# Kernel optimization log

Hardware: AMD Instinct MI355X
Metric: run time of the kernel (lower is better)

Reference implementation:

```python
import jax, jax.numpy as jnp
import numpy as np

N_HEADS = 16
EMBD = 1024
D_HEAD = EMBD // N_HEADS

def setup_inputs() -> dict:
    key = jax.random.key(0)
    ks = jax.random.split(key, 5)
    x = jax.random.normal(ks[0], (2, 2048, EMBD), dtype=jnp.float32)
    # Linear weights stored torch-style [out, in]; apply as x @ W.T + b
    W_in = jax.random.normal(ks[1], (3 * EMBD, EMBD), dtype=jnp.float32) * (EMBD ** -0.5)
    b_in = jax.random.normal(ks[2], (3 * EMBD,), dtype=jnp.float32) * 0.01
    W_out = jax.random.normal(ks[3], (EMBD, EMBD), dtype=jnp.float32) * (EMBD ** -0.5)
    b_out = jax.random.normal(ks[4], (EMBD,), dtype=jnp.float32) * 0.01
    return {"x": x, "W_in": W_in, "b_in": b_in, "W_out": W_out, "b_out": b_out}

def reference(x, W_in, b_in, W_out, b_out):
    B, S, D = x.shape
    qkv = x @ W_in.T + b_in                      # [B, S, 3D]
    q, k, v = jnp.split(qkv, 3, axis=-1)
    def heads(t):
        return t.reshape(B, S, N_HEADS, D_HEAD).transpose(0, 2, 1, 3)  # [B,H,S,d]
    q, k, v = heads(q), heads(k), heads(v)
    scale = 1.0 / jnp.sqrt(jnp.float32(D_HEAD))
    scores = jnp.einsum('bhqd,bhkd->bhqk', q, k) * scale
    weights = jax.nn.softmax(scores, axis=-1)
    out = jnp.einsum('bhqk,bhkd->bhqd', weights, v)  # [B,H,S,d]
    out = out.transpose(0, 2, 1, 3).reshape(B, S, D)
    return out @ W_out.T + b_out
```

## Files before the change

### kernel.cpp

```cpp
#include <hip/hip_runtime.h>
#include <cstdint>

#define EMBD 1024
#define NH 16
#define DH 64
#define BB 2
#define SS 2048
#define M_TOT (BB*SS)
#define N_QKV (3*EMBD)

typedef __bf16 bf16_t;
typedef bf16_t bf16x8 __attribute__((ext_vector_type(8)));
typedef float f32x4 __attribute__((ext_vector_type(4)));
typedef unsigned short u16;
typedef unsigned int u32;

static __device__ __forceinline__ u16 f2bf(float f) {
    union { float f; unsigned u; } c; c.f = f;
    unsigned u = c.u;
    unsigned r = (u + 0x7FFFu + ((u >> 16) & 1u)) >> 16;
    return (u16)r;
}

#define GLDS16(gp, lp) \
    __builtin_amdgcn_global_load_lds((const __attribute__((address_space(1))) void*)(gp), \
                                     (__attribute__((address_space(3))) void*)(lp), 16, 0, 0)

#define NX8 (M_TOT * EMBD / 8)
#define NWI8 (N_QKV * EMBD / 8)
#define NWO8 (EMBD * EMBD / 8)
__global__ void cast_all(const float* __restrict__ x, const float* __restrict__ wi,
                         const float* __restrict__ wo, u16* __restrict__ xb,
                         u16* __restrict__ wib, u16* __restrict__ wob) {
    int i = blockIdx.x * blockDim.x + threadIdx.x;
    const float* s; u16* d; int off;
    if (i < NX8)              { s = x;  d = xb;  off = i; }
    else if (i < NX8 + NWI8)  { s = wi; d = wib; off = i - NX8; }
    else                      { s = wo; d = wob; off = i - NX8 - NWI8; }
    const float4* s4 = (const float4*)s;
    float4 a = s4[2 * off];
    float4 b = s4[2 * off + 1];
    union { u16 u[8]; uint4 v; } r;
    r.u[0] = f2bf(a.x); r.u[1] = f2bf(a.y); r.u[2] = f2bf(a.z); r.u[3] = f2bf(a.w);
    r.u[4] = f2bf(b.x); r.u[5] = f2bf(b.y); r.u[6] = f2bf(b.z); r.u[7] = f2bf(b.w);
    ((uint4*)d)[off] = r.v;
}

#define QSCALE (0.125f * 1.4426950408889634f)
__global__ __launch_bounds__(256) void gemm_qkv(
    const u16* __restrict__ Xb,
    const u16* __restrict__ Wb,
    const float* __restrict__ b_in,
    u16* __restrict__ Q, u16* __restrict__ Kf, u16* __restrict__ Vpf)
{
    __shared__ u16 AB[3][8192];
    const int t = threadIdx.x;
    const int lane = t & 63;
    const int wave = t >> 6;
    const int wm = wave >> 1, wn = wave & 1;
    const int quad = lane >> 4, l16 = lane & 15;
    const int m0 = blockIdx.y * 128, n0 = blockIdx.x * 128;

    const int s0i = t, s1i = 256 + t;
    const u16* ga0 = Xb + (size_t)(m0 + (s0i >> 2)) * EMBD + (s0i & 3) * 8;
    const u16* ga1 = Xb + (size_t)(m0 + (s1i >> 2)) * EMBD + (s1i & 3) * 8;
    const u16* gb0 = Wb + (size_t)(n0 + (s0i >> 2)) * EMBD + (s0i & 3) * 8;
    const u16* gb1 = Wb + (size_t)(n0 + (s1i >> 2)) * EMBD + (s1i & 3) * 8;

    f32x4 acc[4][4] = {};

#pragma unroll
    for (int p = 0; p < 2; ++p) {
        u16* buf = &AB[p][0];
        GLDS16(ga0 + p * 32, buf + s0i * 8);
        GLDS16(ga1 + p * 32, buf + s1i * 8);
        GLDS16(gb0 + p * 32, buf + 4096 + s0i * 8);
        GLDS16(gb1 + p * 32, buf + 4096 + s1i * 8);
    }

    int bi = 0;
    int bw = 2;
    for (int it = 0; it < EMBD / 32; ++it) {
        asm volatile("s_waitcnt vmcnt(4)" ::: "memory");
        __syncthreads();
        {
            int k0 = (it + 2) * 32;
            u16* buf = &AB[bw][0];
            GLDS16(ga0 + k0, buf + s0i * 8);
            GLDS16(ga1 + k0, buf + s1i * 8);
            GLDS16(gb0 + k0, buf + 4096 + s0i * 8);
            GLDS16(gb1 + k0, buf + 4096 + s1i * 8);
        }
        const u16* As = &AB[bi][0];
        const u16* Bs = &AB[bi][4096];
        bf16x8 af[4], bfr[4];
#pragma unroll
        for (int im = 0; im < 4; ++im)
            af[im] = *(const bf16x8*)(As + (wm * 64 + im * 16 + l16) * 32 + quad * 8);
#pragma unroll
        for (int in = 0; in < 4; ++in)
            bfr[in] = *(const bf16x8*)(Bs + (wn * 64 + in * 16 + l16) * 32 + quad * 8);
#pragma unroll
        for (int im = 0; im < 4; ++im)
#pragma unroll
            for (int in = 0; in < 4; ++in)
                acc[im][in] = __builtin_amdgcn_mfma_f32_16x16x32_bf16(
                    af[im], bfr[in], acc[im][in], 0, 0, 0);
        bi = (bi == 2) ? 0 : bi + 1;
        bw = (bw == 2) ? 0 : bw + 1;
    }

#pragma unroll
    for (int im = 0; im < 4; ++im) {
        int rbase = m0 + wm * 64 + im * 16 + quad * 4;
        int b = rbase >> 11, ss = rbase & (SS - 1);
#pragma unroll
        for (int in = 0; in < 4; ++in) {
            int col = n0 + wn * 64 + in * 16 + l16;
            float bias = b_in[col];
            float v0 = acc[im][in][0] + bias;
            float v1 = acc[im][in][1] + bias;
            float v2 = acc[im][in][2] + bias;
            float v3 = acc[im][in][3] + bias;
            if (col < EMBD) {
                int h = col >> 6, d = col & 63;
                u16* qp = Q + (((size_t)(b * NH + h) * SS) + ss) * DH + d;
                qp[0]      = f2bf(v0 * QSCALE);
                qp[DH]     = f2bf(v1 * QSCALE);
                qp[2 * DH] = f2bf(v2 * QSCALE);
                qp[3 * DH] = f2bf(v3 * QSCALE);
            } else if (col < 2 * EMBD) {
                int c = col - EMBD; int h = c >> 6, d = c & 63;
                u16* kp = Kf + (size_t)(b * NH + h) * SS * DH
                          + (ss >> 4) * 1024 + (d >> 5) * 512
                          + (ss & 15) * 32 + ((d >> 3) & 3) * 8 + (d & 7);
                kp[0]  = f2bf(v0);
                kp[32] = f2bf(v1);
                kp[64] = f2bf(v2);
                kp[96] = f2bf(v3);
            } else {
                int c = col - 2 * EMBD; int h = c >> 6, d = c & 63;
                int p32 = ((ss >> 2) & 3) * 8 + ((ss >> 4) & 1) * 4;
                u32 lo = (u32)f2bf(v0) | ((u32)f2bf(v1) << 16);
                u32 hi = (u32)f2bf(v2) | ((u32)f2bf(v3) << 16);
                uint2 pk; pk.x = lo; pk.y = hi;
                *(uint2*)(Vpf + (size_t)(b * NH + h) * SS * DH
                          + (ss >> 5) * 2048 + (d >> 4) * 512 + (d & 15) * 32 + p32) = pk;
            }
        }
    }
}

#define OST 72
__global__ __launch_bounds__(256, 2) void attn(
    const u16* __restrict__ Q, const u16* __restrict__ Kf,
    const u16* __restrict__ Vpf, u16* __restrict__ AO)
{
    __shared__ u16 KV[2][16384];
    const int t = threadIdx.x;
    const int lane = t & 63, w = t >> 6;
    const int quad = lane >> 4, l16 = lane & 15;
    const int b0 = blockIdx.x;
    const int bh = (b0 & 7) * 4 + ((b0 >> 3) & 3);
    const int qt = b0 >> 5;
    const int q0 = qt * 128 + w * 32;

    const u16* Qh = Q + ((size_t)bh * SS + q0) * DH;
    const u16* Kh = Kf + (size_t)bh * SS * DH;
    const u16* Vh = Vpf + (size_t)bh * SS * DH;

    bf16x8 qb[2][2];
#pragma unroll
    for (int qi = 0; qi < 2; ++qi) {
        qb[qi][0] = *(const bf16x8*)(Qh + (qi * 16 + l16) * DH + quad * 8);
        qb[qi][1] = *(const bf16x8*)(Qh + (qi * 16 + l16) * DH + 32 + quad * 8);
    }

    f32x4 o[2][4] = {};
    float lsum[2] = {0.f, 0.f};

#pragma unroll
    for (int i = 0; i < 4; ++i) {
        GLDS16(Kh + i * 2048 + t * 8, &KV[0][0] + i * 2048 + t * 8);
        GLDS16(Vh + i * 2048 + t * 8, &KV[0][8192] + i * 2048 + t * 8);
    }

    for (int it = 0; it < SS / 128; ++it) {
        asm volatile("s_waitcnt vmcnt(0)" ::: "memory");
        __syncthreads();
        if (it + 1 < SS / 128) {
            const u16* kc = Kh + (it + 1) * 8192;
            const u16* vc = Vh + (it + 1) * 8192;
            u16* kb = &KV[(it + 1) & 1][0];
            u16* vb = &KV[(it + 1) & 1][8192];
#pragma unroll
            for (int i = 0; i < 4; ++i) {
                GLDS16(kc + i * 2048 + t * 8, kb + i * 2048 + t * 8);
                GLDS16(vc + i * 2048 + t * 8, vb + i * 2048 + t * 8);
            }
        }
        const u16* Kb = &KV[it & 1][0];
        const u16* Vb = &KV[it & 1][8192];
#pragma unroll
        for (int g = 0; g < 4; ++g) {
            bf16x8 ka00 = *(const bf16x8*)(Kb + (2 * g) * 1024 +       l16 * 32 + quad * 8);
            bf16x8 ka01 = *(const bf16x8*)(Kb + (2 * g) * 1024 + 512 + l16 * 32 + quad * 8);
            bf16x8 ka10 = *(const bf16x8*)(Kb + (2 * g + 1) * 1024 +       l16 * 32 + quad * 8);
            bf16x8 ka11 = *(const bf16x8*)(Kb + (2 * g + 1) * 1024 + 512 + l16 * 32 + quad * 8);
            bf16x8 va0 = *(const bf16x8*)(Vb + g * 2048 +        l16 * 32 + quad * 8);
            bf16x8 va1 = *(const bf16x8*)(Vb + g * 2048 + 512  + l16 * 32 + quad * 8);
            bf16x8 va2 = *(const bf16x8*)(Vb + g * 2048 + 1024 + l16 * 32 + quad * 8);
            bf16x8 va3 = *(const bf16x8*)(Vb + g * 2048 + 1536 + l16 * 32 + quad * 8);
            bf16x8 pb[2];
#pragma unroll
            for (int qi = 0; qi < 2; ++qi) {
                f32x4 z0 = {0.f, 0.f, 0.f, 0.f};
                f32x4 z1 = {0.f, 0.f, 0.f, 0.f};
                z0 = __builtin_amdgcn_mfma_f32_16x16x32_bf16(ka00, qb[qi][0], z0, 0, 0, 0);
                z0 = __builtin_amdgcn_mfma_f32_16x16x32_bf16(ka01, qb[qi][1], z0, 0, 0, 0);
                z1 = __builtin_amdgcn_mfma_f32_16x16x32_bf16(ka10, qb[qi][0], z1, 0, 0, 0);
                z1 = __builtin_amdgcn_mfma_f32_16x16x32_bf16(ka11, qb[qi][1], z1, 0, 0, 0);
                u32 ue[8];
                float ls = 0.f;
#pragma unroll
                for (int j = 0; j < 4; ++j) {
                    float e0 = __builtin_amdgcn_exp2f(z0[j]);
                    float e1 = __builtin_amdgcn_exp2f(z1[j]);
                    ls += e0 + e1;
                    union { float f; u32 v; } c0, c1;
                    c0.f = e0; c1.f = e1;
                    ue[j] = c0.v + 0x8000u;
                    ue[4 + j] = c1.v + 0x8000u;
                }
                lsum[qi] += ls;
                union { uint4 u; bf16x8 b; } cv;
                cv.u.x = __builtin_amdgcn_perm(ue[1], ue[0], 0x07060302u);
                cv.u.y = __builtin_amdgcn_perm(ue[3], ue[2], 0x07060302u);
                cv.u.z = __builtin_amdgcn_perm(ue[5], ue[4], 0x07060302u);
                cv.u.w = __builtin_amdgcn_perm(ue[7], ue[6], 0x07060302u);
                pb[qi] = cv.b;
            }
            o[0][0] = __builtin_amdgcn_mfma_f32_16x16x32_bf16(va0, pb[0], o[0][0], 0, 0, 0);
            o[0][1] = __builtin_amdgcn_mfma_f32_16x16x32_bf16(va1, pb[0], o[0][1], 0, 0, 0);
            o[0][2] = __builtin_amdgcn_mfma_f32_16x16x32_bf16(va2, pb[0], o[0][2], 0, 0, 0);
            o[0][3] = __builtin_amdgcn_mfma_f32_16x16x32_bf16(va3, pb[0], o[0][3], 0, 0, 0);
            o[1][0] = __builtin_amdgcn_mfma_f32_16x16x32_bf16(va0, pb[1], o[1][0], 0, 0, 0);
            o[1][1] = __builtin_amdgcn_mfma_f32_16x16x32_bf16(va1, pb[1], o[1][1], 0, 0, 0);
            o[1][2] = __builtin_amdgcn_mfma_f32_16x16x32_bf16(va2, pb[1], o[1][2], 0, 0, 0);
            o[1][3] = __builtin_amdgcn_mfma_f32_16x16x32_bf16(va3, pb[1], o[1][3], 0, 0, 0);
        }
    }

    float rl[2];
#pragma unroll
    for (int qi = 0; qi < 2; ++qi) {
        float v = lsum[qi];
        v += __shfl_xor(v, 16, 64);
        v += __shfl_xor(v, 32, 64);
        rl[qi] = 1.0f / v;
    }
    __syncthreads();
    u16* Ksc = &KV[0][0];
#pragma unroll
    for (int qi = 0; qi < 2; ++qi)
#pragma unroll
        for (int dt = 0; dt < 4; ++dt)
#pragma unroll
            for (int jj = 0; jj < 2; ++jj) {
                u32 lo_ = (u32)f2bf(o[qi][dt][2 * jj] * rl[qi]);
                u32 hi_ = (u32)f2bf(o[qi][dt][2 * jj + 1] * rl[qi]);
                *(u32*)(Ksc + (w * 32 + qi * 16 + l16) * OST + dt * 16 + quad * 4 + jj * 2) =
                    lo_ | (hi_ << 16);
            }
    __syncthreads();
    const int b = bh >> 4, h = bh & 15;
#pragma unroll
    for (int i = 0; i < 4; ++i) {
        int idx = i * 256 + t;
        int q = idx >> 3, c = idx & 7;
        uint4 vv = *(const uint4*)(Ksc + q * OST + c * 8);
        *(uint4*)(AO + ((size_t)(b * SS + qt * 128 + q)) * EMBD + h * DH + c * 8) = vv;
    }
}

__global__ __launch_bounds__(256) void gemm_out(
    const u16* __restrict__ Ab,
    const u16* __restrict__ Wb,
    const float* __restrict__ b_out,
    float* __restrict__ Out)
{
    __shared__ u16 AB[3][8192];
    const int t = threadIdx.x;
    const int lane = t & 63;
    const int wave = t >> 6;
    const int wm = wave >> 1, wn = wave & 1;
    const int quad = lane >> 4, l16 = lane & 15;
    const int m0 = blockIdx.y * 128, n0 = blockIdx.x * 128;

    const int s0i = t, s1i = 256 + t;
    const u16* ga0 = Ab + (size_t)(m0 + (s0i >> 2)) * EMBD + (s0i & 3) * 8;
    const u16* ga1 = Ab + (size_t)(m0 + (s1i >> 2)) * EMBD + (s1i & 3) * 8;
    const u16* gb0 = Wb + (size_t)(n0 + (s0i >> 2)) * EMBD + (s0i & 3) * 8;
    const u16* gb1 = Wb + (size_t)(n0 + (s1i >> 2)) * EMBD + (s1i & 3) * 8;

    f32x4 acc[4][4] = {};

#pragma unroll
    for (int p = 0; p < 2; ++p) {
        u16* buf = &AB[p][0];
        GLDS16(ga0 + p * 32, buf + s0i * 8);
        GLDS16(ga1 + p * 32, buf + s1i * 8);
        GLDS16(gb0 + p * 32, buf + 4096 + s0i * 8);
        GLDS16(gb1 + p * 32, buf + 4096 + s1i * 8);
    }

    int bi = 0, bw = 2;
    for (int it = 0; it < EMBD / 32; ++it) {
        asm volatile("s_waitcnt vmcnt(4)" ::: "memory");
        __syncthreads();
        {
            int k0 = (it + 2) * 32;
            u16* buf = &AB[bw][0];
            GLDS16(ga0 + k0, buf + s0i * 8);
            GLDS16(ga1 + k0, buf + s1i * 8);
            GLDS16(gb0 + k0, buf + 4096 + s0i * 8);
            GLDS16(gb1 + k0, buf + 4096 + s1i * 8);
        }
        const u16* As = &AB[bi][0];
        const u16* Bs = &AB[bi][4096];
        bf16x8 af[4], bfr[4];
#pragma unroll
        for (int im = 0; im < 4; ++im)
            af[im] = *(const bf16x8*)(As + (wm * 64 + im * 16 + l16) * 32 + quad * 8);
#pragma unroll
        for (int in = 0; in < 4; ++in)
            bfr[in] = *(const bf16x8*)(Bs + (wn * 64 + in * 16 + l16) * 32 + quad * 8);
#pragma unroll
        for (int im = 0; im < 4; ++im)
#pragma unroll
            for (int in = 0; in < 4; ++in)
                acc[im][in] = __builtin_amdgcn_mfma_f32_16x16x32_bf16(
                    af[im], bfr[in], acc[im][in], 0, 0, 0);
        bi = (bi == 2) ? 0 : bi + 1;
        bw = (bw == 2) ? 0 : bw + 1;
    }

#pragma unroll
    for (int im = 0; im < 4; ++im) {
        int rbase = m0 + wm * 64 + im * 16 + quad * 4;
#pragma unroll
        for (int in = 0; in < 4; ++in) {
            int col = n0 + wn * 64 + in * 16 + l16;
            float bias = b_out[col];
#pragma unroll
            for (int j = 0; j < 4; ++j)
                Out[(size_t)(rbase + j) * EMBD + col] = acc[im][in][j] + bias;
        }
    }
}

extern "C" void kernel_launch(void* const* d_in, const int* in_sizes, int n_in,
                              void* d_out, int out_size, void* d_ws, size_t ws_size,
                              hipStream_t stream)
{
    (void)in_sizes; (void)n_in; (void)out_size; (void)ws_size;
    const float* x     = (const float*)d_in[0];
    const float* W_in  = (const float*)d_in[1];
    const float* b_in  = (const float*)d_in[2];
    const float* W_out = (const float*)d_in[3];
    const float* b_out = (const float*)d_in[4];
    float* out = (float*)d_out;

    char* ws = (char*)d_ws;
    u16* xb  = (u16*)(ws);
    u16* wib = (u16*)(ws + 8u  * 1024 * 1024);
    u16* wob = (u16*)(ws + 14u * 1024 * 1024);
    u16* Qw  = (u16*)(ws + 16u * 1024 * 1024);
    u16* Kw  = (u16*)(ws + 24u * 1024 * 1024);
    u16* Vpw = (u16*)(ws + 32u * 1024 * 1024);
    u16* AO  = (u16*)(ws + 40u * 1024 * 1024);

    cast_all<<<(NX8 + NWI8 + NWO8) / 256, 256, 0, stream>>>(x, W_in, W_out, xb, wib, wob);
    gemm_qkv<<<dim3(N_QKV / 128, M_TOT / 128), 256, 0, stream>>>(xb, wib, b_in, Qw, Kw, Vpw);
    attn<<<512, 256, 0, stream>>>(Qw, Kw, Vpw, AO);
    gemm_out<<<dim3(EMBD / 128, M_TOT / 128), 256, 0, stream>>>(AO, wob, b_out, out);
}
```

Baseline: 178.8 us.

## Fuse cast, QKV GEMM, attention and output GEMM into one persistent kernel

Replaces the four launches with a single 512-block persistent kernel that runs each stage in turn, separated by a software grid barrier built on an atomic counter. The GEMM tiles are reshaped so every stage maps onto exactly 512 blocks: 128x192 tiles for QKV and 128x64 tiles for the output projection. The GEMM pipelines go from triple to double buffering and now wait for all loads to finish each iteration. The aim is to remove launch gaps and tail effects between stages. The trade-offs are barrier spin cost, smaller output tiles, a shallower prefetch, and a deadlock risk if the 512 blocks are not all resident at once.

```diff
diff --git a/kernel.cpp b/kernel.cpp
--- a/kernel.cpp
+++ b/kernel.cpp
@@ -8,6 +8,8 @@
 #define SS 2048
 #define M_TOT (BB*SS)
 #define N_QKV (3*EMBD)
+#define GRID 512
+#define NTHREADS (GRID*256)
 
 typedef __bf16 bf16_t;
 typedef bf16_t bf16x8 __attribute__((ext_vector_type(8)));
@@ -26,17 +28,30 @@
     __builtin_amdgcn_global_load_lds((const __attribute__((address_space(1))) void*)(gp), \
                                      (__attribute__((address_space(3))) void*)(lp), 16, 0, 0)
 
+__device__ unsigned g_bar = 0;
+static __device__ __forceinline__ void grid_sync() {
+    __syncthreads();
+    if (threadIdx.x == 0) {
+        __threadfence();
+        unsigned old = __hip_atomic_fetch_add(&g_bar, 1u, __ATOMIC_ACQ_REL,
+                                              __HIP_MEMORY_SCOPE_AGENT);
+        unsigned target = (old / GRID + 1u) * GRID;
+        while (__hip_atomic_load(&g_bar, __ATOMIC_ACQUIRE,
+                                 __HIP_MEMORY_SCOPE_AGENT) < target)
+            __builtin_amdgcn_s_sleep(8);
+        __threadfence();
+    }
+    __syncthreads();
+}
+
 #define NX8 (M_TOT * EMBD / 8)
 #define NWI8 (N_QKV * EMBD / 8)
 #define NWO8 (EMBD * EMBD / 8)
-__global__ void cast_all(const float* __restrict__ x, const float* __restrict__ wi,
-                         const float* __restrict__ wo, u16* __restrict__ xb,
-                         u16* __restrict__ wib, u16* __restrict__ wob) {
-    int i = blockIdx.x * blockDim.x + threadIdx.x;
-    const float* s; u16* d; int off;
-    if (i < NX8)              { s = x;  d = xb;  off = i; }
-    else if (i < NX8 + NWI8)  { s = wi; d = wib; off = i - NX8; }
-    else                      { s = wo; d = wob; off = i - NX8 - NWI8; }
+#define QSCALE (0.125f * 1.4426950408889634f)
+#define OST 72
+
+static __device__ __forceinline__ void cast8(const float* __restrict__ s,
+                                             u16* __restrict__ d, int off) {
     const float4* s4 = (const float4*)s;
     float4 a = s4[2 * off];
     float4 b = s4[2 * off + 1];
@@ -46,315 +61,292 @@
     ((uint4*)d)[off] = r.v;
 }
 
-#define QSCALE (0.125f * 1.4426950408889634f)
-__global__ __launch_bounds__(256) void gemm_qkv(
-    const u16* __restrict__ Xb,
-    const u16* __restrict__ Wb,
-    const float* __restrict__ b_in,
-    u16* __restrict__ Q, u16* __restrict__ Kf, u16* __restrict__ Vpf)
+__global__ __launch_bounds__(256, 2) void fused_attn(
+    const float* __restrict__ x, const float* __restrict__ W_in,
+    const float* __restrict__ b_in, const float* __restrict__ W_out,
+    const float* __restrict__ b_out,
+    u16* __restrict__ xb, u16* __restrict__ wib, u16* __restrict__ wob,
+    u16* __restrict__ Q, u16* __restrict__ Kf, u16* __restrict__ Vpf,
+    u16* __restrict__ AO, float* __restrict__ Out)
 {
-    __shared__ u16 AB[3][8192];
+    __shared__ u16 SH[32768];
     const int t = threadIdx.x;
-    const int lane = t & 63;
-    const int wave = t >> 6;
-    const int wm = wave >> 1, wn = wave & 1;
-    const int quad = lane >> 4, l16 = lane & 15;
-    const int m0 = blockIdx.y * 128, n0 = blockIdx.x * 128;
-
-    const int s0i = t, s1i = 256 + t;
-    const u16* ga0 = Xb + (size_t)(m0 + (s0i >> 2)) * EMBD + (s0i & 3) * 8;
-    const u16* ga1 = Xb + (size_t)(m0 + (s1i >> 2)) * EMBD + (s1i & 3) * 8;
-    const u16* gb0 = Wb + (size_t)(n0 + (s0i >> 2)) * EMBD + (s0i & 3) * 8;
-    const u16* gb1 = Wb + (size_t)(n0 + (s1i >> 2)) * EMBD + (s1i & 3) * 8;
-
-    f32x4 acc[4][4] = {};
-
-#pragma unroll
-    for (int p = 0; p < 2; ++p) {
-        u16* buf = &AB[p][0];
-        GLDS16(ga0 + p * 32, buf + s0i * 8);
-        GLDS16(ga1 + p * 32, buf + s1i * 8);
-        GLDS16(gb0 + p * 32, buf + 4096 + s0i * 8);
-        GLDS16(gb1 + p * 32, buf + 4096 + s1i * 8);
-    }
-
-    int bi = 0;
-    int bw = 2;
-    for (int it = 0; it < EMBD / 32; ++it) {
-        asm volatile("s_waitcnt vmcnt(4)" ::: "memory");
-        __syncthreads();
-        {
-            int k0 = (it + 2) * 32;
-            u16* buf = &AB[bw][0];
-            GLDS16(ga0 + k0, buf + s0i * 8);
-            GLDS16(ga1 + k0, buf + s1i * 8);
-            GLDS16(gb0 + k0, buf + 4096 + s0i * 8);
-            GLDS16(gb1 + k0, buf + 4096 + s1i * 8);
-        }
-        const u16* As = &AB[bi][0];
-        const u16* Bs = &AB[bi][4096];
-        bf16x8 af[4], bfr[4];
-#pragma unroll
-        for (int im = 0; im < 4; ++im)
-            af[im] = *(const bf16x8*)(As + (wm * 64 + im * 16 + l16) * 32 + quad * 8);
-#pragma unroll
-        for (int in = 0; in < 4; ++in)
-            bfr[in] = *(const bf16x8*)(Bs + (wn * 64 + in * 16 + l16) * 32 + quad * 8);
-#pragma unroll
-        for (int im = 0; im < 4; ++im)
-#pragma unroll
-            for (int in = 0; in < 4; ++in)
-                acc[im][in] = __builtin_amdgcn_mfma_f32_16x16x32_bf16(
-                    af[im], bfr[in], acc[im][in], 0, 0, 0);
-        bi = (bi == 2) ? 0 : bi + 1;
-        bw = (bw == 2) ? 0 : bw + 1;
-    }
-
-#pragma unroll
-    for (int im = 0; im < 4; ++im) {
-        int rbase = m0 + wm * 64 + im * 16 + quad * 4;
-        int b = rbase >> 11, ss = rbase & (SS - 1);
-#pragma unroll
-        for (int in = 0; in < 4; ++in) {
-            int col = n0 + wn * 64 + in * 16 + l16;
-            float bias = b_in[col];
-            float v0 = acc[im][in][0] + bias;
-            float v1 = acc[im][in][1] + bias;
-            float v2 = acc[im][in][2] + bias;
-            float v3 = acc[im][in][3] + bias;
-            if (col < EMBD) {
-                int h = col >> 6, d = col & 63;
-                u16* qp = Q + (((size_t)(b * NH + h) * SS) + ss) * DH + d;
-                qp[0]      = f2bf(v0 * QSCALE);
-                qp[DH]     = f2bf(v1 * QSCALE);
-                qp[2 * DH] = f2bf(v2 * QSCALE);
-                qp[3 * DH] = f2bf(v3 * QSCALE);
-            } else if (col < 2 * EMBD) {
-                int c = col - EMBD; int h = c >> 6, d = c & 63;
-                u16* kp = Kf + (size_t)(b * NH + h) * SS * DH
-                          + (ss >> 4) * 1024 + (d >> 5) * 512
-                          + (ss & 15) * 32 + ((d >> 3) & 3) * 8 + (d & 7);
-                kp[0]  = f2bf(v0);
-                kp[32] = f2bf(v1);
-                kp[64] = f2bf(v2);
-                kp[96] = f2bf(v3);
-            } else {
-                int c = col - 2 * EMBD; int h = c >> 6, d = c & 63;
-                int p32 = ((ss >> 2) & 3) * 8 + ((ss >> 4) & 1) * 4;
-                u32 lo = (u32)f2bf(v0) | ((u32)f2bf(v1) << 16);
-                u32 hi = (u32)f2bf(v2) | ((u32)f2bf(v3) << 16);
-                uint2 pk; pk.x = lo; pk.y = hi;
-                *(uint2*)(Vpf + (size_t)(b * NH + h) * SS * DH
-                          + (ss >> 5) * 2048 + (d >> 4) * 512 + (d & 15) * 32 + p32) = pk;
-            }
-        }
-    }
-}
-
-#define OST 72
-__global__ __launch_bounds__(256, 2) void attn(
-    const u16* __restrict__ Q, const u16* __restrict__ Kf,
-    const u16* __restrict__ Vpf, u16* __restrict__ AO)
-{
-    __shared__ u16 KV[2][16384];
-    const int t = threadIdx.x;
+    const int bx = blockIdx.x;
     const int lane = t & 63, w = t >> 6;
     const int quad = lane >> 4, l16 = lane & 15;
-    const int b0 = blockIdx.x;
-    const int bh = (b0 & 7) * 4 + ((b0 >> 3) & 3);
-    const int qt = b0 >> 5;
-    const int q0 = qt * 128 + w * 32;
-
-    const u16* Qh = Q + ((size_t)bh * SS + q0) * DH;
-    const u16* Kh = Kf + (size_t)bh * SS * DH;
-    const u16* Vh = Vpf + (size_t)bh * SS * DH;
-
-    bf16x8 qb[2][2];
-#pragma unroll
-    for (int qi = 0; qi < 2; ++qi) {
-        qb[qi][0] = *(const bf16x8*)(Qh + (qi * 16 + l16) * DH + quad * 8);
-        qb[qi][1] = *(const bf16x8*)(Qh + (qi * 16 + l16) * DH + 32 + quad * 8);
-    }
-
-    f32x4 o[2][4] = {};
-    float lsum[2] = {0.f, 0.f};
-
-#pragma unroll
-    for (int i = 0; i < 4; ++i) {
-        GLDS16(Kh + i * 2048 + t * 8, &KV[0][0] + i * 2048 + t * 8);
-        GLDS16(Vh + i * 2048 + t * 8, &KV[0][8192] + i * 2048 + t * 8);
-    }
-
-    for (int it = 0; it < SS / 128; ++it) {
-        asm volatile("s_waitcnt vmcnt(0)" ::: "memory");
+    const int wm = w >> 1, wn = w & 1;
+
+    {
+        int tid = bx * 256 + t;
+        for (int g = tid; g < NX8; g += NTHREADS)  cast8(x, xb, g);
+        for (int g = tid; g < NWI8; g += NTHREADS) cast8(W_in, wib, g);
+        for (int g = tid; g < NWO8; g += NTHREADS) cast8(W_out, wob, g);
+    }
+    grid_sync();
+
+    {
+        const int m0 = (bx >> 4) * 128;
+        const int n0 = (bx & 15) * 192;
+        const int sA0 = t, sA1 = 256 + t;
+        const int sB0 = t, sB1 = 256 + t, sB2 = 512 + t;
+        const u16* gA0 = xb + (size_t)(m0 + (sA0 >> 2)) * EMBD + (sA0 & 3) * 8;
+        const u16* gA1 = xb + (size_t)(m0 + (sA1 >> 2)) * EMBD + (sA1 & 3) * 8;
+        const u16* gB0 = wib + (size_t)(n0 + (sB0 >> 2)) * EMBD + (sB0 & 3) * 8;
+        const u16* gB1 = wib + (size_t)(n0 + (sB1 >> 2)) * EMBD + (sB1 & 3) * 8;
+        const u16* gB2 = wib + (size_t)(n0 + (sB2 >> 2)) * EMBD + (sB2 & 3) * 8;
+
+        f32x4 acc[4][6] = {};
+
+        {
+            u16* buf = SH;
+            GLDS16(gA0, buf + sA0 * 8); GLDS16(gA1, buf + sA1 * 8);
+            GLDS16(gB0, buf + 4096 + sB0 * 8); GLDS16(gB1, buf + 4096 + sB1 * 8);
+            GLDS16(gB2, buf + 4096 + sB2 * 8);
+        }
+        for (int it = 0; it < EMBD / 32; ++it) {
+            asm volatile("s_waitcnt vmcnt(0)" ::: "memory");
+            __syncthreads();
+            if (it + 1 < EMBD / 32) {
+                int k0 = (it + 1) * 32;
+                u16* buf = SH + ((it + 1) & 1) * 10240;
+                GLDS16(gA0 + k0, buf + sA0 * 8); GLDS16(gA1 + k0, buf + sA1 * 8);
+                GLDS16(gB0 + k0, buf + 4096 + sB0 * 8);
+                GLDS16(gB1 + k0, buf + 4096 + sB1 * 8);
+                GLDS16(gB2 + k0, buf + 4096 + sB2 * 8);
+            }
+            const u16* As = SH + (it & 1) * 10240;
+            const u16* Bs = As + 4096;
+            bf16x8 af[4], bfr[6];
+#pragma unroll
+            for (int im = 0; im < 4; ++im)
+                af[im] = *(const bf16x8*)(As + (wm * 64 + im * 16 + l16) * 32 + quad * 8);
+#pragma unroll
+            for (int in = 0; in < 6; ++in)
+                bfr[in] = *(const bf16x8*)(Bs + (wn * 96 + in * 16 + l16) * 32 + quad * 8);
+#pragma unroll
+            for (int im = 0; im < 4; ++im)
+#pragma unroll
+                for (int in = 0; in < 6; ++in)
+                    acc[im][in] = __builtin_amdgcn_mfma_f32_16x16x32_bf16(
+                        af[im], bfr[in], acc[im][in], 0, 0, 0);
+        }
+#pragma unroll
+        for (int im = 0; im < 4; ++im) {
+            int rbase = m0 + wm * 64 + im * 16 + quad * 4;
+            int b = rbase >> 11, ss = rbase & (SS - 1);
+#pragma unroll
+            for (int in = 0; in < 6; ++in) {
+                int col = n0 + wn * 96 + in * 16 + l16;
+                float bias = b_in[col];
+                float v0 = acc[im][in][0] + bias;
+                float v1 = acc[im][in][1] + bias;
+                float v2 = acc[im][in][2] + bias;
+                float v3 = acc[im][in][3] + bias;
+                if (col < EMBD) {
+                    int h = col >> 6, d = col & 63;
+                    u16* qp = Q + (((size_t)(b * NH + h) * SS) + ss) * DH + d;
+                    qp[0]      = f2bf(v0 * QSCALE);
+                    qp[DH]     = f2bf(v1 * QSCALE);
+                    qp[2 * DH] = f2bf(v2 * QSCALE);
+                    qp[3 * DH] = f2bf(v3 * QSCALE);
+                } else if (col < 2 * EMBD) {
+                    int c = col - EMBD; int h = c >> 6, d = c & 63;
+                    u16* kp = Kf + (size_t)(b * NH + h) * SS * DH
+                              + (ss >> 4) * 1024 + (d >> 5) * 512
+                              + (ss & 15) * 32 + ((d >> 3) & 3) * 8 + (d & 7);
+                    kp[0]  = f2bf(v0);
+                    kp[32] = f2bf(v1);
+                    kp[64] = f2bf(v2);
+                    kp[96] = f2bf(v3);
+                } else {
+                    int c = col - 2 * EMBD; int h = c >> 6, d = c & 63;
+                    int p32 = ((ss >> 2) & 3) * 8 + ((ss >> 4) & 1) * 4;
+                    u32 lo = (u32)f2bf(v0) | ((u32)f2bf(v1) << 16);
+                    u32 hi = (u32)f2bf(v2) | ((u32)f2bf(v3) << 16);
+                    uint2 pk; pk.x = lo; pk.y = hi;
+                    *(uint2*)(Vpf + (size_t)(b * NH + h) * SS * DH
+                              + (ss >> 5) * 2048 + (d >> 4) * 512 + (d & 15) * 32 + p32) = pk;
+                }
+            }
+        }
+    }
+    grid_sync();
+
+    {
+        const int bh = (bx & 7) * 4 + ((bx >> 3) & 3);
+        const int qt = bx >> 5;
+        const int q0 = qt * 128 + w * 32;
+
+        const u16* Qh = Q + ((size_t)bh * SS + q0) * DH;
+        const u16* Kh = Kf + (size_t)bh * SS * DH;
+        const u16* Vh = Vpf + (size_t)bh * SS * DH;
+
+        bf16x8 qb[2][2];
+#pragma unroll
+        for (int qi = 0; qi < 2; ++qi) {
+            qb[qi][0] = *(const bf16x8*)(Qh + (qi * 16 + l16) * DH + quad * 8);
+            qb[qi][1] = *(const bf16x8*)(Qh + (qi * 16 + l16) * DH + 32 + quad * 8);
+        }
+
+        f32x4 o[2][4] = {};
+        float lsum[2] = {0.f, 0.f};
+
+#pragma unroll
+        for (int i = 0; i < 4; ++i) {
+            GLDS16(Kh + i * 2048 + t * 8, SH + i * 2048 + t * 8);
+            GLDS16(Vh + i * 2048 + t * 8, SH + 8192 + i * 2048 + t * 8);
+        }
+
+        for (int it = 0; it < SS / 128; ++it) {
+            asm volatile("s_waitcnt vmcnt(0)" ::: "memory");
+            __syncthreads();
+            if (it + 1 < SS / 128) {
+                const u16* kc = Kh + (it + 1) * 8192;
+                const u16* vc = Vh + (it + 1) * 8192;
+                u16* kb = SH + ((it + 1) & 1) * 16384;
+                u16* vb = kb + 8192;
+#pragma unroll
+                for (int i = 0; i < 4; ++i) {
+                    GLDS16(kc + i * 2048 + t * 8, kb + i * 2048 + t * 8);
+                    GLDS16(vc + i * 2048 + t * 8, vb + i * 2048 + t * 8);
+                }
+            }
+            const u16* Kb = SH + (it & 1) * 16384;
+            const u16* Vb = Kb + 8192;
+#pragma unroll
+            for (int g = 0; g < 4; ++g) {
+                bf16x8 ka00 = *(const bf16x8*)(Kb + (2 * g) * 1024 +       l16 * 32 + quad * 8);
+                bf16x8 ka01 = *(const bf16x8*)(Kb + (2 * g) * 1024 + 512 + l16 * 32 + quad * 8);
+                bf16x8 ka10 = *(const bf16x8*)(Kb + (2 * g + 1) * 1024 +       l16 * 32 + quad * 8);
+                bf16x8 ka11 = *(const bf16x8*)(Kb + (2 * g + 1) * 1024 + 512 + l16 * 32 + quad * 8);
+                bf16x8 va0 = *(const bf16x8*)(Vb + g * 2048 +        l16 * 32 + quad * 8);
+                bf16x8 va1 = *(const bf16x8*)(Vb + g * 2048 + 512  + l16 * 32 + quad * 8);
+                bf16x8 va2 = *(const bf16x8*)(Vb + g * 2048 + 1024 + l16 * 32 + quad * 8);
+                bf16x8 va3 = *(const bf16x8*)(Vb + g * 2048 + 1536 + l16 * 32 + quad * 8);
+                bf16x8 pb[2];
+#pragma unroll
+                for (int qi = 0; qi < 2; ++qi) {
+                    f32x4 z0 = {0.f, 0.f, 0.f, 0.f};
+                    f32x4 z1 = {0.f, 0.f, 0.f, 0.f};
+                    z0 = __builtin_amdgcn_mfma_f32_16x16x32_bf16(ka00, qb[qi][0], z0, 0, 0, 0);
+                    z0 = __builtin_amdgcn_mfma_f32_16x16x32_bf16(ka01, qb[qi][1], z0, 0, 0, 0);
+                    z1 = __builtin_amdgcn_mfma_f32_16x16x32_bf16(ka10, qb[qi][0], z1, 0, 0, 0);
+                    z1 = __builtin_amdgcn_mfma_f32_16x16x32_bf16(ka11, qb[qi][1], z1, 0, 0, 0);
+                    u32 ue[8];
+                    float ls = 0.f;
+#pragma unroll
+                    for (int j = 0; j < 4; ++j) {
+                        float e0 = __builtin_amdgcn_exp2f(z0[j]);
+                        float e1 = __builtin_amdgcn_exp2f(z1[j]);
+                        ls += e0 + e1;
+                        union { float f; u32 v; } c0, c1;
+                        c0.f = e0; c1.f = e1;
+                        ue[j] = c0.v + 0x8000u;
+                        ue[4 + j] = c1.v + 0x8000u;
+                    }
+                    lsum[qi] += ls;
+                    union { uint4 u; bf16x8 b; } cv;
+                    cv.u.x = __builtin_amdgcn_perm(ue[1], ue[0], 0x07060302u);
+                    cv.u.y = __builtin_amdgcn_perm(ue[3], ue[2], 0x07060302u);
+                    cv.u.z = __builtin_amdgcn_perm(ue[5], ue[4], 0x07060302u);
+                    cv.u.w = __builtin_amdgcn_perm(ue[7], ue[6], 0x07060302u);
+                    pb[qi] = cv.b;
+                }
+                o[0][0] = __builtin_amdgcn_mfma_f32_16x16x32_bf16(va0, pb[0], o[0][0], 0, 0, 0);
+                o[0][1] = __builtin_amdgcn_mfma_f32_16x16x32_bf16(va1, pb[0], o[0][1], 0, 0, 0);
+                o[0][2] = __builtin_amdgcn_mfma_f32_16x16x32_bf16(va2, pb[0], o[0][2], 0, 0, 0);
+                o[0][3] = __builtin_amdgcn_mfma_f32_16x16x32_bf16(va3, pb[0], o[0][3], 0, 0, 0);
+                o[1][0] = __builtin_amdgcn_mfma_f32_16x16x32_bf16(va0, pb[1], o[1][0], 0, 0, 0);
+                o[1][1] = __builtin_amdgcn_mfma_f32_16x16x32_bf16(va1, pb[1], o[1][1], 0, 0, 0);
+                o[1][2] = __builtin_amdgcn_mfma_f32_16x16x32_bf16(va2, pb[1], o[1][2], 0, 0, 0);
+                o[1][3] = __builtin_amdgcn_mfma_f32_16x16x32_bf16(va3, pb[1], o[1][3], 0, 0, 0);
+            }
+        }
+
+        float rl[2];
+#pragma unroll
+        for (int qi = 0; qi < 2; ++qi) {
+            float v = lsum[qi];
+            v += __shfl_xor(v, 16, 64);
+            v += __shfl_xor(v, 32, 64);
+            rl[qi] = 1.0f / v;
+        }
         __syncthreads();
-        if (it + 1 < SS / 128) {
-            const u16* kc = Kh + (it + 1) * 8192;
-            const u16* vc = Vh + (it + 1) * 8192;
-            u16* kb = &KV[(it + 1) & 1][0];
-            u16* vb = &KV[(it + 1) & 1][8192];
-#pragma unroll
-            for (int i = 0; i < 4; ++i) {
-                GLDS16(kc + i * 2048 + t * 8, kb + i * 2048 + t * 8);
-                GLDS16(vc + i * 2048 + t * 8, vb + i * 2048 + t * 8);
-            }
-        }
-        const u16* Kb = &KV[it & 1][0];
-        const u16* Vb = &KV[it & 1][8192];
-#pragma unroll
-        for (int g = 0; g < 4; ++g) {
-            bf16x8 ka00 = *(const bf16x8*)(Kb + (2 * g) * 1024 +       l16 * 32 + quad * 8);
-            bf16x8 ka01 = *(const bf16x8*)(Kb + (2 * g) * 1024 + 512 + l16 * 32 + quad * 8);
-            bf16x8 ka10 = *(const bf16x8*)(Kb + (2 * g + 1) * 1024 +       l16 * 32 + quad * 8);
-            bf16x8 ka11 = *(const bf16x8*)(Kb + (2 * g + 1) * 1024 + 512 + l16 * 32 + quad * 8);
-            bf16x8 va0 = *(const bf16x8*)(Vb + g * 2048 +        l16 * 32 + quad * 8);
-            bf16x8 va1 = *(const bf16x8*)(Vb + g * 2048 + 512  + l16 * 32 + quad * 8);
-            bf16x8 va2 = *(const bf16x8*)(Vb + g * 2048 + 1024 + l16 * 32 + quad * 8);
-            bf16x8 va3 = *(const bf16x8*)(Vb + g * 2048 + 1536 + l16 * 32 + quad * 8);
-            bf16x8 pb[2];
-#pragma unroll
-            for (int qi = 0; qi < 2; ++qi) {
-                f32x4 z0 = {0.f, 0.f, 0.f, 0.f};
-                f32x4 z1 = {0.f, 0.f, 0.f, 0.f};
-                z0 = __builtin_amdgcn_mfma_f32_16x16x32_bf16(ka00, qb[qi][0], z0, 0, 0, 0);
-                z0 = __builtin_amdgcn_mfma_f32_16x16x32_bf16(ka01, qb[qi][1], z0, 0, 0, 0);
-                z1 = __builtin_amdgcn_mfma_f32_16x16x32_bf16(ka10, qb[qi][0], z1, 0, 0, 0);
-                z1 = __builtin_amdgcn_mfma_f32_16x16x32_bf16(ka11, qb[qi][1], z1, 0, 0, 0);
-                u32 ue[8];
-                float ls = 0.f;
-#pragma unroll
-                for (int j = 0; j < 4; ++j) {
-                    float e0 = __builtin_amdgcn_exp2f(z0[j]);
-                    float e1 = __builtin_amdgcn_exp2f(z1[j]);
-                    ls += e0 + e1;
-                    union { float f; u32 v; } c0, c1;
-                    c0.f = e0; c1.f = e1;
-                    ue[j] = c0.v + 0x8000u;
-                    ue[4 + j] = c1.v + 0x8000u;
+#pragma unroll
+        for (int qi = 0; qi < 2; ++qi)
+#pragma unroll
+            for (int dt = 0; dt < 4; ++dt)
+#pragma unroll
+                for (int jj = 0; jj < 2; ++jj) {
+                    u32 lo_ = (u32)f2bf(o[qi][dt][2 * jj] * rl[qi]);
+                    u32 hi_ = (u32)f2bf(o[qi][dt][2 * jj + 1] * rl[qi]);
+                    *(u32*)(SH + (w * 32 + qi * 16 + l16) * OST + dt * 16 + quad * 4 + jj * 2) =
+                        lo_ | (hi_ << 16);
                 }
-                lsum[qi] += ls;
-                union { uint4 u; bf16x8 b; } cv;
-                cv.u.x = __builtin_amdgcn_perm(ue[1], ue[0], 0x07060302u);
-                cv.u.y = __builtin_amdgcn_perm(ue[3], ue[2], 0x07060302u);
-                cv.u.z = __builtin_amdgcn_perm(ue[5], ue[4], 0x07060302u);
-                cv.u.w = __builtin_amdgcn_perm(ue[7], ue[6], 0x07060302u);
-                pb[qi] = cv.b;
-            }
-            o[0][0] = __builtin_amdgcn_mfma_f32_16x16x32_bf16(va0, pb[0], o[0][0], 0, 0, 0);
-            o[0][1] = __builtin_amdgcn_mfma_f32_16x16x32_bf16(va1, pb[0], o[0][1], 0, 0, 0);
-            o[0][2] = __builtin_amdgcn_mfma_f32_16x16x32_bf16(va2, pb[0], o[0][2], 0, 0, 0);
-            o[0][3] = __builtin_amdgcn_mfma_f32_16x16x32_bf16(va3, pb[0], o[0][3], 0, 0, 0);
-            o[1][0] = __builtin_amdgcn_mfma_f32_16x16x32_bf16(va0, pb[1], o[1][0], 0, 0, 0);
-            o[1][1] = __builtin_amdgcn_mfma_f32_16x16x32_bf16(va1, pb[1], o[1][1], 0, 0, 0);
-            o[1][2] = __builtin_amdgcn_mfma_f32_16x16x32_bf16(va2, pb[1], o[1][2], 0, 0, 0);
-            o[1][3] = __builtin_amdgcn_mfma_f32_16x16x32_bf16(va3, pb[1], o[1][3], 0, 0, 0);
-        }
-    }
-
-    float rl[2];
-#pragma unroll
-    for (int qi = 0; qi < 2; ++qi) {
-        float v = lsum[qi];
-        v += __shfl_xor(v, 16, 64);
-        v += __shfl_xor(v, 32, 64);
-        rl[qi] = 1.0f / v;
-    }
-    __syncthreads();
-    u16* Ksc = &KV[0][0];
-#pragma unroll
-    for (int qi = 0; qi < 2; ++qi)
-#pragma unroll
-        for (int dt = 0; dt < 4; ++dt)
-#pragma unroll
-            for (int jj = 0; jj < 2; ++jj) {
-                u32 lo_ = (u32)f2bf(o[qi][dt][2 * jj] * rl[qi]);
-                u32 hi_ = (u32)f2bf(o[qi][dt][2 * jj + 1] * rl[qi]);
-                *(u32*)(Ksc + (w * 32 + qi * 16 + l16) * OST + dt * 16 + quad * 4 + jj * 2) =
-                    lo_ | (hi_ << 16);
-            }
-    __syncthreads();
-    const int b = bh >> 4, h = bh & 15;
-#pragma unroll
-    for (int i = 0; i < 4; ++i) {
-        int idx = i * 256 + t;
-        int q = idx >> 3, c = idx & 7;
-        uint4 vv = *(const uint4*)(Ksc + q * OST + c * 8);
-        *(uint4*)(AO + ((size_t)(b * SS + qt * 128 + q)) * EMBD + h * DH + c * 8) = vv;
-    }
-}
-
-__global__ __launch_bounds__(256) void gemm_out(
-    const u16* __restrict__ Ab,
-    const u16* __restrict__ Wb,
-    const float* __restrict__ b_out,
-    float* __restrict__ Out)
-{
-    __shared__ u16 AB[3][8192];
-    const int t = threadIdx.x;
-    const int lane = t & 63;
-    const int wave = t >> 6;
-    const int wm = wave >> 1, wn = wave & 1;
-    const int quad = lane >> 4, l16 = lane & 15;
-    const int m0 = blockIdx.y * 128, n0 = blockIdx.x * 128;
-
-    const int s0i = t, s1i = 256 + t;
-    const u16* ga0 = Ab + (size_t)(m0 + (s0i >> 2)) * EMBD + (s0i & 3) * 8;
-    const u16* ga1 = Ab + (size_t)(m0 + (s1i >> 2)) * EMBD + (s1i & 3) * 8;
-    const u16* gb0 = Wb + (size_t)(n0 + (s0i >> 2)) * EMBD + (s0i & 3) * 8;
-    const u16* gb1 = Wb + (size_t)(n0 + (s1i >> 2)) * EMBD + (s1i & 3) * 8;
-
-    f32x4 acc[4][4] = {};
-
-#pragma unroll
-    for (int p = 0; p < 2; ++p) {
-        u16* buf = &AB[p][0];
-        GLDS16(ga0 + p * 32, buf + s0i * 8);
-        GLDS16(ga1 + p * 32, buf + s1i * 8);
-        GLDS16(gb0 + p * 32, buf + 4096 + s0i * 8);
-        GLDS16(gb1 + p * 32, buf + 4096 + s1i * 8);
-    }
-
-    int bi = 0, bw = 2;
-    for (int it = 0; it < EMBD / 32; ++it) {
-        asm volatile("s_waitcnt vmcnt(4)" ::: "memory");
         __syncthreads();
+        const int b = bh >> 4, h = bh & 15;
+#pragma unroll
+        for (int i = 0; i < 4; ++i) {
+            int idx = i * 256 + t;
+            int q = idx >> 3, c = idx & 7;
+            uint4 vv = *(const uint4*)(SH + q * OST + c * 8);
+            *(uint4*)(AO + ((size_t)(b * SS + qt * 128 + q)) * EMBD + h * DH + c * 8) = vv;
+        }
+    }
+    grid_sync();
+
+    {
+        const int m0 = (bx >> 4) * 128;
+        const int n0 = (bx & 15) * 64;
+        const int sA0 = t, sA1 = 256 + t;
+        const int sB0 = t;
+        const u16* gA0 = AO + (size_t)(m0 + (sA0 >> 2)) * EMBD + (sA0 & 3) * 8;
+        const u16* gA1 = AO + (size_t)(m0 + (sA1 >> 2)) * EMBD + (sA1 & 3) * 8;
+        const u16* gB0 = wob + (size_t)(n0 + (sB0 >> 2)) * EMBD + (sB0 & 3) * 8;
+
+        f32x4 acc[4][2] = {};
+
         {
-            int k0 = (it + 2) * 32;
-            u16* buf = &AB[bw][0];
-            GLDS16(ga0 + k0, buf + s0i * 8);
-            GLDS16(ga1 + k0, buf + s1i * 8);
-            GLDS16(gb0 + k0, buf + 4096 + s0i * 8);
-            GLDS16(gb1 + k0, buf + 4096 + s1i * 8);
-        }
-        const u16* As = &AB[bi][0];
-        const u16* Bs = &AB[bi][4096];
-        bf16x8 af[4], bfr[4];
-#pragma unroll
-        for (int im = 0; im < 4; ++im)
-            af[im] = *(const bf16x8*)(As + (wm * 64 + im * 16 + l16) * 32 + quad * 8);
-#pragma unroll
-        for (int in = 0; in < 4; ++in)
-            bfr[in] = *(const bf16x8*)(Bs + (wn * 64 + in * 16 + l16) * 32 + quad * 8);
-#pragma unroll
-        for (int im = 0; im < 4; ++im)
-#pragma unroll
-            for (int in = 0; in < 4; ++in)
-                acc[im][in] = __builtin_amdgcn_mfma_f32_16x16x32_bf16(
-                    af[im], bfr[in], acc[im][in], 0, 0, 0);
-        bi = (bi == 2) ? 0 : bi + 1;
-        bw = (bw == 2) ? 0 : bw + 1;
-    }
-
-#pragma unroll
-    for (int im = 0; im < 4; ++im) {
-        int rbase = m0 + wm * 64 + im * 16 + quad * 4;
-#pragma unroll
-        for (int in = 0; in < 4; ++in) {
-            int col = n0 + wn * 64 + in * 16 + l16;
-            float bias = b_out[col];
-#pragma unroll
-            for (int j = 0; j < 4; ++j)
-                Out[(size_t)(rbase + j) * EMBD + col] = acc[im][in][j] + bias;
+            u16* buf = SH;
+            GLDS16(gA0, buf + sA0 * 8); GLDS16(gA1, buf + sA1 * 8);
+            GLDS16(gB0, buf + 4096 + sB0 * 8);
+        }
+        for (int it = 0; it < EMBD / 32; ++it) {
+            asm volatile("s_waitcnt vmcnt(0)" ::: "memory");
+            __syncthreads();
+            if (it + 1 < EMBD / 32) {
+                int k0 = (it + 1) * 32;
+                u16* buf = SH + ((it + 1) & 1) * 8192;
+                GLDS16(gA0 + k0, buf + sA0 * 8); GLDS16(gA1 + k0, buf + sA1 * 8);
+                GLDS16(gB0 + k0, buf + 4096 + sB0 * 8);
+            }
+            const u16* As = SH + (it & 1) * 8192;
+            const u16* Bs = As + 4096;
+            bf16x8 af[4], bfr[2];
+#pragma unroll
+            for (int im = 0; im < 4; ++im)
+                af[im] = *(const bf16x8*)(As + (wm * 64 + im * 16 + l16) * 32 + quad * 8);
+#pragma unroll
+            for (int in = 0; in < 2; ++in)
+                bfr[in] = *(const bf16x8*)(Bs + (wn * 32 + in * 16 + l16) * 32 + quad * 8);
+#pragma unroll
+            for (int im = 0; im < 4; ++im)
+#pragma unroll
+                for (int in = 0; in < 2; ++in)
+                    acc[im][in] = __builtin_amdgcn_mfma_f32_16x16x32_bf16(
+                        af[im], bfr[in], acc[im][in], 0, 0, 0);
+        }
+#pragma unroll
+        for (int im = 0; im < 4; ++im) {
+            int rbase = m0 + wm * 64 + im * 16 + quad * 4;
+#pragma unroll
+            for (int in = 0; in < 2; ++in) {
+                int col = n0 + wn * 32 + in * 16 + l16;
+                float bias = b_out[col];
+#pragma unroll
+                for (int j = 0; j < 4; ++j)
+                    Out[(size_t)(rbase + j) * EMBD + col] = acc[im][in][j] + bias;
+            }
         }
     }
 }
@@ -380,8 +372,6 @@
     u16* Vpw = (u16*)(ws + 32u * 1024 * 1024);
     u16* AO  = (u16*)(ws + 40u * 1024 * 1024);
 
-    cast_all<<<(NX8 + NWI8 + NWO8) / 256, 256, 0, stream>>>(x, W_in, W_out, xb, wib, wob);
-    gemm_qkv<<<dim3(N_QKV / 128, M_TOT / 128), 256, 0, stream>>>(xb, wib, b_in, Qw, Kw, Vpw);
-    attn<<<512, 256, 0, stream>>>(Qw, Kw, Vpw, AO);
-    gemm_out<<<dim3(EMBD / 128, M_TOT / 128), 256, 0, stream>>>(AO, wob, b_out, out);
-}
+    fused_attn<<<GRID, 256, 0, stream>>>(x, W_in, b_in, W_out, b_out,
+                                         xb, wib, wob, Qw, Kw, Vpw, AO, out);
+}
```

After: 392.3 us. 2.19x slower.
